# Kernel optimization log

Measured on AMD Instinct MI355X. Metric: run time of the kernel, lower is better.

Reference implementation:

```python
import jax, jax.numpy as jnp
import numpy as np

B, G, GI = 128, 360, 174          # batch, n_groups, voxels per group
EF, ET, U = 512, 512, 512         # feat embed, text embed, LSTM units
AU, VOC, T = 32, 5000, 20         # attention units, vocab, max_len


def _leaky(x):
    return jnp.where(x >= 0, x, 0.2 * x)


def _ln(x, g, b, eps=1e-5):
    m = x.mean(-1, keepdims=True)
    v = ((x - m) ** 2).mean(-1, keepdims=True)
    return (x - m) / jnp.sqrt(v + eps) * g + b


def setup_inputs() -> dict:
    key = jax.random.key(0)
    ks = jax.random.split(key, 24)
    def n(k, shape, s=0.02):
        return jax.random.normal(k, shape, jnp.float32) * s
    return {
        "features": jax.random.normal(ks[0], (B, G * GI), jnp.float32),
        "text": jax.random.randint(ks[1], (B, T), 0, VOC),
        "a0": jnp.zeros((B, U), jnp.float32),
        "c0": jnp.zeros((B, U), jnp.float32),
        "enc_W": n(ks[2], (G, GI, EF)), "enc_b": n(ks[3], (G, EF)),
        "enc_ln_g": jnp.ones((EF,), jnp.float32), "enc_ln_b": jnp.zeros((EF,), jnp.float32),
        "attn_W1": n(ks[4], (EF, AU)), "attn_b1": n(ks[5], (AU,)),
        "attn_W2": n(ks[6], (U, AU)), "attn_b2": n(ks[7], (AU,)),
        "attn_V": n(ks[8], (AU, 1)), "attn_bV": n(ks[9], (1,)),
        "emb": n(ks[10], (VOC, ET)),
        "W_ih": n(ks[11], (4 * U, EF + ET)), "W_hh": n(ks[12], (4 * U, U)),
        "b_ih": n(ks[13], (4 * U,)), "b_hh": n(ks[14], (4 * U,)),
        "ln_g": jnp.ones((U,), jnp.float32), "ln_b": jnp.zeros((U,), jnp.float32),
        "dec_W1": n(ks[15], (U, 256)), "dec_b1": n(ks[16], (256,)),
        "dec_W2": n(ks[17], (256, VOC)), "dec_b2": n(ks[18], (VOC,)),
        "subject": 0,
    }


def reference(features, text, a0, c0, enc_W, enc_b, enc_ln_g, enc_ln_b,
              attn_W1, attn_b1, attn_W2, attn_b2, attn_V, attn_bV, emb,
              W_ih, W_hh, b_ih, b_hh, ln_g, ln_b,
              dec_W1, dec_b1, dec_W2, dec_b2, subject):
    # LocallyConnected encoder (weights for the selected subject): groups are
    # 360 contiguous equal splits of the voxel axis -> gather == reshape.
    x = features.reshape(B, G, GI)
    feat = _ln(_leaky(jnp.einsum('bgi,gio->bgo', x, enc_W) + enc_b),
               enc_ln_g, enc_ln_b)                       # [B, G, EF]
    # hidden-independent half of attention, hoisted out of the recurrence
    f1 = jax.nn.relu(jnp.einsum('bge,eu->bgu', feat, attn_W1) + attn_b1)  # [B,G,AU]
    txt = emb[text]                                      # [B, T, ET]

    def step(carry, x_t):
        a, c = carry                                     # [B,U], [B,U]
        h2 = jax.nn.relu(a @ attn_W2 + attn_b2)          # [B, AU]
        score = jnp.tanh(f1 + h2[:, None, :]) @ attn_V + attn_bV  # [B,G,1]
        w = jax.nn.softmax(score, axis=1)
        ctx = jnp.sum(w * feat, axis=1)                  # [B, EF]
        xin = jnp.concatenate([ctx, x_t], axis=1)        # [B, EF+ET]
        gates = xin @ W_ih.T + a @ W_hh.T + b_ih + b_hh  # [B, 4U]
        i, f, g, o = jnp.split(gates, 4, axis=1)         # torch gate order i,f,g,o
        c = jax.nn.sigmoid(f) * c + jax.nn.sigmoid(i) * jnp.tanh(g)
        h = jax.nn.sigmoid(o) * jnp.tanh(c)
        a = _ln(_leaky(h), ln_g, ln_b)                   # fed back as LSTM hidden
        out = jax.nn.softmax(_leaky(a @ dec_W1 + dec_b1) @ dec_W2 + dec_b2, axis=-1)
        return (a, c), (out, w)

    _, (outs, ws) = jax.lax.scan(step, (a0, c0), jnp.swapaxes(txt, 0, 1))
    output = jnp.swapaxes(outs, 0, 1)                    # [B, T, VOC]
    attention_scores = jnp.swapaxes(ws, 0, 1)            # [B, T, G, 1]
    return output, attention_scores
```

## Files before the change

### kernel.cpp

```cpp
#include <hip/hip_runtime.h>
#include <stdint.h>

#define B_  128
#define G_  360
#define GI_ 174
#define EF_ 512
#define U_  512
#define AU_ 32
#define VOC_ 5000
#define T_  20

typedef short short8 __attribute__((ext_vector_type(8)));
typedef float floatx4 __attribute__((ext_vector_type(4)));

#define GLD16(gp, lp) __builtin_amdgcn_global_load_lds( \
    (const __attribute__((address_space(1))) void*)(gp), \
    (__attribute__((address_space(3))) void*)(lp), 16, 0, 0)

__device__ __forceinline__ unsigned short f2bf(float f){
  unsigned u = __float_as_uint(f);
  u += 0x7fffu + ((u>>16)&1u);
  return (unsigned short)(u>>16);
}
__device__ __forceinline__ float2 bfpair(unsigned u){
  float2 r; r.x = __uint_as_float(u<<16); r.y = __uint_as_float(u & 0xffff0000u); return r;
}
__device__ __forceinline__ unsigned packbf(float a, float b){
  return ((unsigned)f2bf(b)<<16) | (unsigned)f2bf(a);
}
__device__ __forceinline__ float sigmf(float x){ return 1.0f/(1.0f + __expf(-x)); }
__device__ __forceinline__ float tanhf_(float x){ return 1.0f - 2.0f/(1.0f + __expf(2.0f*x)); }
__device__ __forceinline__ float leaky_(float x){ return x >= 0.f ? x : 0.2f*x; }

__device__ __forceinline__ int swzcol(int cc, int e){
  return (cc & ~63) | ((((cc>>3)&7) ^ e)<<3) | (cc&7);
}

__global__ __launch_bounds__(256) void k_cvt(
    const int* __restrict__ text, const float* __restrict__ emb,
    const float* __restrict__ Wih, const float* __restrict__ Whh,
    const float* __restrict__ bih, const float* __restrict__ bhh,
    const float* __restrict__ W1, const float* __restrict__ b1,
    const float* __restrict__ encg, const float* __restrict__ encb,
    const float* __restrict__ dW1, const float* __restrict__ dW2,
    float* __restrict__ stats, unsigned short* __restrict__ Wstep,
    float* __restrict__ bias_sum, unsigned short* __restrict__ ASbuf,
    unsigned short* __restrict__ W1g, float* __restrict__ f1c,
    unsigned short* __restrict__ dW1t, unsigned short* __restrict__ dW2t)
{
  __shared__ float tile[64][65];
  const int blk = blockIdx.x, tid = threadIdx.x;
  if (blk < 90){
    int i = blk*1024 + tid*4;
    *(float4*)&stats[i] = make_float4(0.f,0.f,0.f,0.f);
  } else if (blk < 2138){
    int j = blk - 90;
    #pragma unroll
    for (int q=0;q<6;++q){
      int c = q*256 + tid;
      float v;
      if (c < 512)       v = Wih[(size_t)j*1024 + 512 + c];
      else if (c < 1024) v = Wih[(size_t)j*1024 + (c - 512)];
      else               v = Whh[(size_t)j*512 + (c - 1024)];
      int cd = c;
      if (c >= 512) cd = 512 + swzcol(c - 512, j&7);
      Wstep[(size_t)j*1536 + cd] = f2bf(v);
    }
  } else if (blk < 2146){
    int i = (blk-2138)*256 + tid;
    bias_sum[i] = bih[i] + bhh[i];
  } else if (blk < 4706){
    int r = blk - 2146; int t = r >> 7, b = r & 127;
    int idx = text[b*T_ + t];
    float2 v = *(const float2*)&emb[(size_t)idx*512 + 2*tid];
    ((unsigned*)ASbuf)[(((size_t)r*1536)>>1) + tid] = packbf(v.x, v.y);
  } else if (blk == 4706){
    if (tid < 32){
      float gw = 0.f, bw = 0.f;
      for (int k=0;k<512;++k){
        float wv = W1[(size_t)k*32 + tid];
        float gk = encg[k], bk = encb[k];
        W1g[(size_t)tid*512 + k] = f2bf(gk*wv);
        gw += gk*wv; bw += bk*wv;
      }
      f1c[tid] = gw; f1c[32+tid] = bw + b1[tid];
    }
  } else if (blk < 4739){
    int q = blk - 4707; int kt = q >> 2, nt = q & 3;
    int k0 = kt*64, n0 = nt*64;
    #pragma unroll
    for (int it=0; it<16; ++it){
      int idx = it*256 + tid; int kk = idx>>6, nn = idx&63;
      tile[kk][nn] = dW1[(size_t)(k0+kk)*256 + n0+nn];
    }
    __syncthreads();
    #pragma unroll
    for (int it=0; it<16; ++it){
      int idx = it*256 + tid; int nn = idx>>6, kk = idx&63;
      dW1t[(size_t)(n0+nn)*512 + k0+kk] = f2bf(tile[kk][nn]);
    }
  } else {
    int q = blk - 4739; int kt = q/80, nt = q - kt*80;
    int k0 = kt*64, n0 = nt*64;
    #pragma unroll
    for (int it=0; it<16; ++it){
      int idx = it*256 + tid; int kk = idx>>6, nn = idx&63;
      tile[kk][nn] = (n0+nn < VOC_) ? dW2[(size_t)(k0+kk)*VOC_ + n0+nn] : 0.f;
    }
    __syncthreads();
    #pragma unroll
    for (int it=0; it<16; ++it){
      int idx = it*256 + tid; int nn = idx>>6, kk = idx&63;
      dW2t[(size_t)(n0+nn)*256 + k0+kk] = f2bf(tile[kk][nn]);
    }
  }
}

__device__ __forceinline__ int swz64(int row, int k){
  return row*64 + ((((k>>3) ^ (row&7)))<<3) + (k&7);
}
__global__ __launch_bounds__(512) void k_enc(
    const float* __restrict__ features, const float* __restrict__ encW,
    const float* __restrict__ encB,
    unsigned short* __restrict__ ybuf, float* __restrict__ stats)
{
  __shared__ __align__(16) unsigned short As[128*64];
  __shared__ __align__(16) unsigned short Bs[128*64];
  const int g = blockIdx.y, n0 = blockIdx.x*128;
  const int tid = threadIdx.x, w = tid>>6, l = tid&63;
  const int quad = l>>4, col16 = l&15;
  const int wm = w>>1, wn = w&1;
  const int m0w = wm*32, n0w = wn*64;

  floatx4 acc[2][4];
  #pragma unroll
  for (int mi=0;mi<2;++mi)
    #pragma unroll
    for (int ni=0;ni<4;++ni)
      acc[mi][ni] = (floatx4){0.f,0.f,0.f,0.f};

  for (int c=0; c<3; ++c){
    if (c > 0) __syncthreads();
    #pragma unroll
    for (int q=0; q<4; ++q){
      int idx = q*512 + tid;
      int row = idx >> 4;
      int kl  = (idx & 15)*4;
      int kgl = c*64 + kl;
      const float* fp = features + (size_t)row*(G_*GI_) + (size_t)g*GI_ + kgl;
      float4 v;
      if (kgl + 3 < GI_){
        v = *(const float4*)fp;
      } else {
        v.x = (kgl+0 < GI_) ? fp[0] : 0.f;
        v.y = (kgl+1 < GI_) ? fp[1] : 0.f;
        v.z = (kgl+2 < GI_) ? fp[2] : 0.f;
        v.w = (kgl+3 < GI_) ? fp[3] : 0.f;
      }
      int e = row*64 + (((kl>>3) ^ (row&7))<<3) + (kl&7);
      uint2 pk; pk.x = packbf(v.x, v.y); pk.y = packbf(v.z, v.w);
      *(uint2*)&As[e] = pk;
    }
    #pragma unroll
    for (int z=0; z<8; ++z){
      int kk = (tid>>6) + 8*z;
      int k  = c*64 + kk;
      int nn = (tid&63)*2;
      if (k < GI_){
        const float* wp = encW + ((size_t)g*GI_ + k)*512 + n0 + nn;
        float2 v = *(const float2*)wp;
        Bs[swz64(nn,   kk)] = f2bf(v.x);
        Bs[swz64(nn+1, kk)] = f2bf(v.y);
      } else {
        Bs[swz64(nn,   kk)] = 0;
        Bs[swz64(nn+1, kk)] = 0;
      }
    }
    __syncthreads();
    #pragma unroll
    for (int it=0; it<2; ++it){
      int kk = it*32 + quad*8;
      short8 af[2], bfr[4];
      #pragma unroll
      for (int mi=0;mi<2;++mi){
        int row = m0w + mi*16 + col16;
        af[mi] = *(const short8*)&As[row*64 + (((kk>>3) ^ (row&7))<<3)];
      }
      #pragma unroll
      for (int ni=0;ni<4;++ni){
        int rowb = n0w + ni*16 + col16;
        bfr[ni] = *(const short8*)&Bs[rowb*64 + (((kk>>3) ^ (rowb&7))<<3)];
      }
      #pragma unroll
      for (int mi=0;mi<2;++mi)
        #pragma unroll
        for (int ni=0;ni<4;++ni)
          acc[mi][ni] = __builtin_amdgcn_mfma_f32_16x16x32_bf16(af[mi], bfr[ni], acc[mi][ni], 0,0,0);
    }
  }

  #pragma unroll
  for (int mi=0;mi<2;++mi){
    float sy[4] = {0.f,0.f,0.f,0.f};
    float sq[4] = {0.f,0.f,0.f,0.f};
    #pragma unroll
    for (int ni=0;ni<4;++ni){
      int nG = n0 + n0w + ni*16 + col16;
      float bv = encB[(size_t)g*512 + nG];
      #pragma unroll
      for (int reg=0;reg<4;++reg){
        int row = m0w + mi*16 + quad*4 + reg;
        float y = leaky_(acc[mi][ni][reg] + bv);
        unsigned short yh = f2bf(y);
        ybuf[((size_t)row*G_ + g)*512 + nG] = yh;
        float yr = __uint_as_float(((unsigned)yh)<<16);
        sy[reg] += yr; sq[reg] += yr*yr;
      }
    }
    #pragma unroll
    for (int reg=0; reg<4; ++reg){
      float a = sy[reg], bq = sq[reg];
      #pragma unroll
      for (int mk=1; mk<16; mk<<=1){ a += __shfl_xor(a, mk, 64); bq += __shfl_xor(bq, mk, 64); }
      if (col16 == 0){
        int row = m0w + mi*16 + quad*4 + reg;
        atomicAdd(&stats[((size_t)row*G_ + g)*2],     a);
        atomicAdd(&stats[((size_t)row*G_ + g)*2 + 1], bq);
      }
    }
  }
}

template<int TN, int NBK, int MODE, int KSPLIT=1>
__global__ __launch_bounds__(256) void k_gemm(
    const unsigned short* __restrict__ A, int lda,
    const unsigned short* __restrict__ Bt, int ldb,
    const float* __restrict__ bias,
    float* __restrict__ outf, unsigned short* __restrict__ outh,
    const float* __restrict__ stats, float* __restrict__ stats2,
    const float* __restrict__ f1c)
{
  constexpr int NI = TN/32;
  __shared__ __align__(16) unsigned short As[128*64];
  __shared__ __align__(16) unsigned short Bs[TN*64];
  const int tid = threadIdx.x;
  const int w = tid >> 6, l = tid & 63;
  const int n0 = blockIdx.x * TN;
  const int ks = (KSPLIT > 1) ? blockIdx.y : 0;
  const int r0 = (KSPLIT > 1) ? 0 : blockIdx.y * 128;
  const int quad = l>>4, col16 = l&15;
  const int m0w = (w>>1)*64, n0w = (w&1)*(TN/2);
  const int arow = w*32, brow = w*(TN/4);

  const unsigned short* Ag = A + (size_t)(r0 + arow + (l>>3))*lda + (l&7)*8;
  const unsigned short* Bg = Bt + (size_t)(n0 + brow + (l>>3))*ldb + (l&7)*8;

  floatx4 acc[4][NI];
  #pragma unroll
  for (int mi=0;mi<4;++mi)
    #pragma unroll
    for (int ni=0;ni<NI;++ni)
      acc[mi][ni] = (floatx4){0.f,0.f,0.f,0.f};

  for (int it=0; it<NBK; ++it){
    int k0 = (ks*NBK + it)*64;
    #pragma unroll
    for (int q=0;q<4;++q)
      GLD16(Ag + (size_t)q*8*lda + k0, As + (arow + q*8)*64);
    #pragma unroll
    for (int q=0;q<TN/32;++q)
      GLD16(Bg + (size_t)q*8*ldb + k0, Bs + (brow + q*8)*64);
    __syncthreads();
    #pragma unroll
    for (int kc=0;kc<2;++kc){
      int koff = kc*32 + quad*8;
      short8 af[4], bfr[NI];
      #pragma unroll
      for (int mi=0;mi<4;++mi)
        af[mi] = *(const short8*)&As[(m0w + mi*16 + col16)*64 + koff];
      #pragma unroll
      for (int ni=0;ni<NI;++ni)
        bfr[ni] = *(const short8*)&Bs[(n0w + ni*16 + col16)*64 + koff];
      #pragma unroll
      for (int mi=0;mi<4;++mi)
        #pragma unroll
        for (int ni=0;ni<NI;++ni)
          acc[mi][ni] = __builtin_amdgcn_mfma_f32_16x16x32_bf16(af[mi], bfr[ni], acc[mi][ni], 0,0,0);
    }
    __syncthreads();
  }

  if constexpr (MODE == 0){
    float* op = outf + (size_t)ks*(128*2048);
    #pragma unroll
    for (int ni=0; ni<NI; ++ni){
      int nG = n0 + n0w + ni*16 + col16;
      float bv = (KSPLIT == 1 || ks == 0) ? bias[nG] : 0.f;
      #pragma unroll
      for (int mi=0; mi<4; ++mi)
        #pragma unroll
        for (int reg=0; reg<4; ++reg){
          int r = r0 + m0w + mi*16 + quad*4 + reg;
          op[(size_t)r*2048 + nG] = acc[mi][ni][reg] + bv;
        }
    }
  } else if constexpr (MODE == 1){
    int nG = n0w + col16;
    float gw = f1c[nG], bwv = f1c[32+nG];
    #pragma unroll
    for (int mi=0; mi<4; ++mi)
      #pragma unroll
      for (int reg=0; reg<4; ++reg){
        int r = r0 + m0w + mi*16 + quad*4 + reg;
        float2 st = *(const float2*)&stats[(size_t)r*2];
        float m = st.x * (1.f/512.f);
        float var = st.y * (1.f/512.f) - m*m;
        float rs = rsqrtf(var + 1e-5f);
        float v = rs*(acc[mi][0][reg] - m*gw) + bwv;
        v = v > 0.f ? v : 0.f;
        outf[(size_t)r*32 + nG] = v;
        if (((w&1)==0) && col16==0){
          stats2[(size_t)r*2] = m; stats2[(size_t)r*2+1] = rs;
        }
      }
  } else if constexpr (MODE == 2){
    #pragma unroll
    for (int ni=0; ni<NI; ++ni){
      int nG = n0 + n0w + ni*16 + col16;
      float bv = bias[nG];
      #pragma unroll
      for (int mi=0; mi<4; ++mi)
        #pragma unroll
        for (int reg=0; reg<4; ++reg){
          int r = r0 + m0w + mi*16 + quad*4 + reg;
          outh[(size_t)r*256 + nG] = f2bf(leaky_(acc[mi][ni][reg] + bv));
        }
    }
  } else {
    #pragma unroll
    for (int ni=0; ni<NI; ++ni){
      int nG = n0 + n0w + ni*16 + col16;
      if (nG < VOC_){
        float bv = bias[nG];
        #pragma unroll
        for (int mi=0; mi<4; ++mi)
          #pragma unroll
          for (int reg=0; reg<4; ++reg){
            int r = r0 + m0w + mi*16 + quad*4 + reg;
            int bb = r & 127, tt = r >> 7;
            outf[((size_t)bb*T_ + tt)*VOC_ + nG] = acc[mi][ni][reg] + bv;
          }
      }
    }
  }
}

__global__ __launch_bounds__(256) void k_gates(
    const unsigned short* __restrict__ A,
    const unsigned short* __restrict__ Bt,
    float* __restrict__ outp)
{
  __shared__ __align__(16) unsigned short As[128*128];
  __shared__ __align__(16) unsigned short Bs[64*128];
  const int tid = threadIdx.x, w = tid>>6, l = tid&63;
  const int ks = blockIdx.y;
  const int n0 = blockIdx.x*64;
  const int quad = l>>4, col16 = l&15;
  const int m0w = (w>>1)*64, n0w = (w&1)*32;
  const int arow = w*32, brow = w*16;

  const unsigned short* Ag = A + (size_t)(arow + (l>>4))*1536 + ks*128 + (l&15)*8;
  const unsigned short* Bg = Bt + (size_t)(n0 + brow + (l>>4))*1536 + 512 + ks*128 + (l&15)*8;
  #pragma unroll
  for (int q=0;q<8;++q)
    GLD16(Ag + (size_t)q*4*1536, As + (arow + q*4)*128);
  #pragma unroll
  for (int q=0;q<4;++q)
    GLD16(Bg + (size_t)q*4*1536, Bs + (brow + q*4)*128);

  floatx4 acc[4][2];
  #pragma unroll
  for (int mi=0;mi<4;++mi)
    #pragma unroll
    for (int ni=0;ni<2;++ni)
      acc[mi][ni] = (floatx4){0.f,0.f,0.f,0.f};

  __syncthreads();
  #pragma unroll
  for (int kc=0;kc<4;++kc){
    int koff = kc*32 + quad*8;
    int kbase = koff & 64;
    int kx = (koff>>3)&7;
    short8 af[4], bfr[2];
    #pragma unroll
    for (int mi=0;mi<4;++mi){
      int row = m0w + mi*16 + col16;
      af[mi] = *(const short8*)&As[row*128 + kbase + ((kx ^ (row&7))<<3)];
    }
    #pragma unroll
    for (int ni=0;ni<2;++ni){
      int rowb = n0w + ni*16 + col16;
      bfr[ni] = *(const short8*)&Bs[rowb*128 + kbase + ((kx ^ (rowb&7))<<3)];
    }
    #pragma unroll
    for (int mi=0;mi<4;++mi)
      #pragma unroll
      for (int ni=0;ni<2;++ni)
        acc[mi][ni] = __builtin_amdgcn_mfma_f32_16x16x32_bf16(af[mi], bfr[ni], acc[mi][ni], 0,0,0);
  }

  float* op = outp + (size_t)ks*(128*2048);
  #pragma unroll
  for (int ni=0; ni<2; ++ni){
    int nG = n0 + n0w + ni*16 + col16;
    #pragma unroll
    for (int mi=0; mi<4; ++mi)
      #pragma unroll
      for (int reg=0; reg<4; ++reg){
        int r = m0w + mi*16 + quad*4 + reg;
        op[(size_t)r*2048 + nG] = acc[mi][ni][reg];
      }
  }
}

__global__ __launch_bounds__(256) void k_cellattn(
    const float* __restrict__ gall, const float* __restrict__ gtx,
    const float* __restrict__ c_in,
    float* __restrict__ c_out, const float* __restrict__ a0,
    const float* __restrict__ lng, const float* __restrict__ lnb,
    const float* __restrict__ W2, const float* __restrict__ b2,
    const float* __restrict__ Vv, const float* __restrict__ bV,
    const float* __restrict__ f1, const unsigned short* __restrict__ ybuf,
    const float* __restrict__ stats2,
    const float* __restrict__ encg, const float* __restrict__ encb,
    unsigned short* __restrict__ ASlot, unsigned short* __restrict__ a_bf,
    float* __restrict__ att_out, int t_att, int mode_cell, int do_attn)
{
  __shared__ float a_s[512];
  __shared__ float sc[G_];
  __shared__ float hred[8*32];
  __shared__ float h2s[32];
  __shared__ float red[16];
  __shared__ float mrs[2];
  __shared__ float2 cred[4][256];
  const int b = blockIdx.x, tid = threadIdx.x;
  const int wv = tid >> 6, ln = tid & 63;

  if (mode_cell){
    float hl2[2];
    #pragma unroll
    for (int q=0;q<2;++q){
      int u = tid + q*256;
      size_t base = (size_t)b*2048;
      float gi = gtx[base+u];
      float gf = gtx[base+512+u];
      float gc = gtx[base+1024+u];
      float go = gtx[base+1536+u];
      #pragma unroll
      for (int s=0;s<8;++s){
        const float* gp = gall + (size_t)s*(128*2048) + base;
        gi += gp[u]; gf += gp[512+u]; gc += gp[1024+u]; go += gp[1536+u];
      }
      float c = sigmf(gf)*c_in[(size_t)b*512+u] + sigmf(gi)*tanhf_(gc);
      c_out[(size_t)b*512+u] = c;
      hl2[q] = leaky_(sigmf(go)*tanhf_(c));
    }
    float s = hl2[0]+hl2[1], ss = hl2[0]*hl2[0]+hl2[1]*hl2[1];
    #pragma unroll
    for (int mk=1;mk<64;mk<<=1){ s += __shfl_xor(s,mk,64); ss += __shfl_xor(ss,mk,64); }
    if (ln==0){ red[wv]=s; red[8+wv]=ss; }
    __syncthreads();
    if (tid==0){
      float S  = red[0]+red[1]+red[2]+red[3];
      float SS = red[8]+red[9]+red[10]+red[11];
      float mean = S*(1.f/512.f);
      float var  = SS*(1.f/512.f) - mean*mean;
      mrs[0]=mean; mrs[1]=rsqrtf(var+1e-5f);
    }
    __syncthreads();
    float mean = mrs[0], rstd = mrs[1];
    #pragma unroll
    for (int q=0;q<2;++q){
      int u = tid + q*256;
      float av = (hl2[q]-mean)*rstd*lng[u] + lnb[u];
      a_s[u] = av;
      a_bf[(size_t)b*512 + u] = f2bf(av);
      if (do_attn){
        int pc = swzcol(512 + u, b&7);
        ASlot[(size_t)b*1536 + 512 + pc] = f2bf(av);
      }
    }
  } else {
    #pragma unroll
    for (int q=0;q<2;++q){
      int u = tid + q*256;
      float av = a0[(size_t)b*512 + u];
      a_s[u] = av;
      int pc = swzcol(512 + u, b&7);
      ASlot[(size_t)b*1536 + 512 + pc] = f2bf(av);
    }
  }
  __syncthreads();
  if (!do_attn) return;

  {
    int u = tid & 31, ch = tid >> 5;
    float p = 0.f;
    const float* w2p = W2 + (size_t)ch*64*32 + u;
    const float* ap = a_s + ch*64;
    #pragma unroll 8
    for (int e=0;e<64;++e) p += ap[e]*w2p[(size_t)e*32];
    hred[ch*32+u] = p;
  }
  __syncthreads();
  if (tid < 32){
    float p = hred[tid];
    #pragma unroll
    for (int ch=1; ch<8; ++ch) p += hred[ch*32+tid];
    p += b2[tid];
    h2s[tid] = p>0.f? p:0.f;
  }
  __syncthreads();
  float bVv = bV[0];
  for (int gg = tid; gg < G_; gg += 256){
    const float* fp = f1 + ((size_t)b*G_ + gg)*32;
    float s = bVv;
    #pragma unroll
    for (int u=0;u<32;++u) s += tanhf_(fp[u] + h2s[u]) * Vv[u];
    sc[gg] = s;
  }
  __syncthreads();
  float mx = -1e30f;
  for (int gg=tid; gg<G_; gg+=256) mx = fmaxf(mx, sc[gg]);
  #pragma unroll
  for (int mk=1;mk<64;mk<<=1) mx = fmaxf(mx, __shfl_xor(mx,mk,64));
  if (ln==0) red[wv]=mx;
  __syncthreads();
  if (tid==0) red[0] = fmaxf(fmaxf(red[0],red[1]),fmaxf(red[2],red[3]));
  __syncthreads();
  mx = red[0];
  float psum = 0.f;
  for (int gg=tid; gg<G_; gg+=256){
    float e = __expf(sc[gg]-mx);
    sc[gg] = e; psum += e;
  }
  #pragma unroll
  for (int mk=1;mk<64;mk<<=1) psum += __shfl_xor(psum,mk,64);
  if (ln==0) red[8+wv]=psum;
  __syncthreads();
  if (tid==0) red[8] = red[8]+red[9]+red[10]+red[11];
  __syncthreads();
  float inv = 1.f/red[8];
  float Mop = 0.f;
  float* wout = att_out + ((size_t)b*T_ + t_att)*G_;
  for (int gg=tid; gg<G_; gg+=256){
    float wg = sc[gg]*inv;
    wout[gg] = wg;
    float2 st = *(const float2*)&stats2[((size_t)b*G_+gg)*2];
    sc[gg] = wg*st.y;
    Mop += wg*st.x*st.y;
  }
  #pragma unroll
  for (int mk=1;mk<64;mk<<=1) Mop += __shfl_xor(Mop,mk,64);
  if (ln==0) red[4+wv] = Mop;
  __syncthreads();
  if (tid==0) mrs[0] = red[4]+red[5]+red[6]+red[7];
  __syncthreads();
  float Mo = mrs[0];
  {
    const unsigned* fp = (const unsigned*)ybuf + ((size_t)b*G_)*256;
    float2 cacc[4];
    #pragma unroll
    for (int k=0;k<4;++k) cacc[k] = make_float2(0.f,0.f);
    int g0 = wv*90;
    for (int gg=g0; gg<g0+90; ++gg){
      float wq = sc[gg];
      #pragma unroll
      for (int k=0;k<4;++k){
        float2 p = bfpair(fp[(size_t)gg*256 + ln + 64*k]);
        cacc[k].x += wq*p.x; cacc[k].y += wq*p.y;
      }
    }
    #pragma unroll
    for (int k=0;k<4;++k) cred[wv][ln + 64*k] = cacc[k];
  }
  __syncthreads();
  {
    float c0v = cred[0][tid].x + cred[1][tid].x + cred[2][tid].x + cred[3][tid].x;
    float c1v = cred[0][tid].y + cred[1][tid].y + cred[2][tid].y + cred[3][tid].y;
    int e0 = 2*tid;
    float ctx0 = encg[e0]  *(c0v - Mo) + encb[e0];
    float ctx1 = encg[e0+1]*(c1v - Mo) + encb[e0+1];
    int pc = swzcol(2*tid, b&7);
    ((unsigned*)ASlot)[((size_t)b*1536 + 512 + pc)>>1] = packbf(ctx0, ctx1);
  }
}

__global__ __launch_bounds__(256) void k_softmax(float* __restrict__ outp)
{
  __shared__ float red[8];
  const size_t row = (size_t)blockIdx.x * VOC_;
  const int tid = threadIdx.x;
  const int wv = tid >> 6, ln = tid & 63;
  float v[20];
  float mx = -1e30f;
  #pragma unroll
  for (int k=0;k<20;++k){
    int idx = tid + k*256;
    v[k] = (idx < VOC_) ? outp[row+idx] : -1e30f;
    mx = fmaxf(mx, v[k]);
  }
  #pragma unroll
  for (int mk=1;mk<64;mk<<=1) mx = fmaxf(mx,__shfl_xor(mx,mk,64));
  if (ln==0) red[wv] = mx;
  __syncthreads();
  if (tid==0) red[0]=fmaxf(fmaxf(red[0],red[1]),fmaxf(red[2],red[3]));
  __syncthreads();
  mx = red[0];
  float s=0.f;
  #pragma unroll
  for (int k=0;k<20;++k){ v[k] = __expf(v[k]-mx); s += v[k]; }
  #pragma unroll
  for (int mk=1;mk<64;mk<<=1) s += __shfl_xor(s,mk,64);
  if (ln==0) red[4+wv]=s;
  __syncthreads();
  if (tid==0) red[4]=red[4]+red[5]+red[6]+red[7];
  __syncthreads();
  float inv = 1.f/red[4];
  #pragma unroll
  for (int k=0;k<20;++k){
    int idx = tid + k*256;
    if (idx < VOC_) outp[row+idx] = v[k]*inv;
  }
}

extern "C" void kernel_launch(void* const* d_in, const int* in_sizes, int n_in,
                              void* d_out, int out_size, void* d_ws, size_t ws_size,
                              hipStream_t stream) {
  const float* features = (const float*)d_in[0];
  const int*   text     = (const int*)d_in[1];
  const float* a0    = (const float*)d_in[2];
  const float* c0    = (const float*)d_in[3];
  const float* encW  = (const float*)d_in[4];
  const float* encB  = (const float*)d_in[5];
  const float* encLNg= (const float*)d_in[6];
  const float* encLNb= (const float*)d_in[7];
  const float* attnW1= (const float*)d_in[8];
  const float* attnb1= (const float*)d_in[9];
  const float* attnW2= (const float*)d_in[10];
  const float* attnb2= (const float*)d_in[11];
  const float* attnV = (const float*)d_in[12];
  const float* attnbV= (const float*)d_in[13];
  const float* emb   = (const float*)d_in[14];
  const float* Wih   = (const float*)d_in[15];
  const float* Whh   = (const float*)d_in[16];
  const float* bih   = (const float*)d_in[17];
  const float* bhh   = (const float*)d_in[18];
  const float* lng   = (const float*)d_in[19];
  const float* lnb   = (const float*)d_in[20];
  const float* dW1   = (const float*)d_in[21];
  const float* db1   = (const float*)d_in[22];
  const float* dW2   = (const float*)d_in[23];
  const float* db2   = (const float*)d_in[24];

  uint8_t* w8 = (uint8_t*)d_ws;
  unsigned short* ybuf   = (unsigned short*)(w8);
  float*          stats  = (float*)(w8 + 47185920);
  float*          stats2 = (float*)(w8 + 47554560);
  float*          f1b    = (float*)(w8 + 47923200);
  unsigned short* ASbuf  = (unsigned short*)(w8 + 53821440);
  unsigned short* Wstep  = (unsigned short*)(w8 + 61685760);
  float*          bias_sum=(float*)(w8 + 67977216);
  unsigned short* W1g    = (unsigned short*)(w8 + 67985408);
  float*          f1c    = (float*)(w8 + 68018176);
  unsigned short* dW1t   = (unsigned short*)(w8 + 68018432);
  unsigned short* dW2t   = (unsigned short*)(w8 + 68280576);
  float*          cws    = (float*)(w8 + 71950592);
  unsigned short* a_bf   = (unsigned short*)(w8 + 72212736);
  unsigned short* d1bf   = (unsigned short*)(w8 + 74834176);

  float* outp = (float*)d_out;
  float* att  = outp + 12800000;
  float* gsplit = outp;
  float* gtxt   = outp + 8*128*2048;

  hipLaunchKernelGGL(k_cvt, dim3(5059), dim3(256), 0, stream,
                     text, emb, Wih, Whh, bih, bhh, attnW1, attnb1,
                     encLNg, encLNb, dW1, dW2,
                     stats, Wstep, bias_sum, ASbuf, W1g, f1c, dW1t, dW2t);
  hipLaunchKernelGGL(k_enc, dim3(4,360), dim3(512), 0, stream,
                     features, encW, encB, ybuf, stats);
  hipLaunchKernelGGL((k_gemm<64,8,0>), dim3(32,20), dim3(256), 0, stream,
                     ASbuf, 1536, Wstep, 1536, bias_sum,
                     gtxt, (unsigned short*)nullptr,
                     (const float*)nullptr, (float*)nullptr, (const float*)nullptr);
  hipLaunchKernelGGL((k_gemm<32,8,1>), dim3(1,360), dim3(256), 0, stream,
                     ybuf, 512, W1g, 512, (const float*)nullptr,
                     f1b, (unsigned short*)nullptr, stats, stats2, f1c);
  hipLaunchKernelGGL(k_cellattn, dim3(128), dim3(256), 0, stream,
                     gsplit, gtxt, c0, cws, a0, lng, lnb, attnW2, attnb2, attnV, attnbV,
                     f1b, ybuf, stats2, encLNg, encLNb,
                     ASbuf, a_bf, att, 0, 0, 1);
  for (int t=0; t<T_; ++t){
    hipLaunchKernelGGL(k_gates, dim3(32,8), dim3(256), 0, stream,
                       ASbuf + (size_t)t*128*1536 + 512, Wstep, gsplit);
    int da = (t < T_-1) ? 1 : 0;
    unsigned short* slot = ASbuf + (size_t)((t+1 < T_) ? (t+1) : 0)*128*1536;
    hipLaunchKernelGGL(k_cellattn, dim3(128), dim3(256), 0, stream,
                       gsplit, gtxt + (size_t)t*128*2048, (t==0)?c0:cws, cws, a0, lng, lnb,
                       attnW2, attnb2, attnV, attnbV,
                       f1b, ybuf, stats2, encLNg, encLNb,
                       slot, a_bf + (size_t)t*128*512, att, t+1, 1, da);
  }
  hipLaunchKernelGGL((k_gemm<128,8,2>), dim3(2,20), dim3(256), 0, stream,
                     a_bf, 512, dW1t, 512, db1,
                     (float*)nullptr, d1bf, (const float*)nullptr, (float*)nullptr,
                     (const float*)nullptr);
  hipLaunchKernelGGL((k_gemm<128,4,3>), dim3(40,20), dim3(256), 0, stream,
                     d1bf, 256, dW2t, 256, db2,
                     outp, (unsigned short*)nullptr, (const float*)nullptr,
                     (float*)nullptr, (const float*)nullptr);
  hipLaunchKernelGGL(k_softmax, dim3(2560), dim3(256), 0, stream, outp);
}
```

Baseline: 1.011 ms.

## Vectorize weight conversion and retile encoder GEMM into smaller 64x64 blocks

The weight-packing section of the conversion kernel now has each thread load eight floats with float4 loads and store them as one 16-byte bf16 vector, with the swizzle applied per 8-element chunk. This cuts that section from 2048 blocks to 256. The encoder GEMM moves from 128x128 tiles with 512 threads to 64x64 tiles with 256 threads, launching 16x360 blocks instead of 4x360, to raise occupancy and parallelism. The cost is that each features and weight element is loaded and converted more times across blocks, and more atomic stat updates are issued.

```diff
diff --git a/kernel.cpp b/kernel.cpp
--- a/kernel.cpp
+++ b/kernel.cpp
@@ -53,28 +53,43 @@
   if (blk < 90){
     int i = blk*1024 + tid*4;
     *(float4*)&stats[i] = make_float4(0.f,0.f,0.f,0.f);
-  } else if (blk < 2138){
-    int j = blk - 90;
-    #pragma unroll
-    for (int q=0;q<6;++q){
-      int c = q*256 + tid;
-      float v;
-      if (c < 512)       v = Wih[(size_t)j*1024 + 512 + c];
-      else if (c < 1024) v = Wih[(size_t)j*1024 + (c - 512)];
-      else               v = Whh[(size_t)j*512 + (c - 1024)];
-      int cd = c;
-      if (c >= 512) cd = 512 + swzcol(c - 512, j&7);
-      Wstep[(size_t)j*1536 + cd] = f2bf(v);
-    }
-  } else if (blk < 2146){
-    int i = (blk-2138)*256 + tid;
+  } else if (blk < 346){
+    int j = (blk - 90)*8 + (tid >> 5);
+    int e = j & 7;
+    #pragma unroll
+    for (int z=0; z<6; ++z){
+      int c0 = ((tid & 31) + 32*z)*8;
+      float4 v0, v1;
+      if (c0 < 512){
+        v0 = *(const float4*)&Wih[(size_t)j*1024 + 512 + c0];
+        v1 = *(const float4*)&Wih[(size_t)j*1024 + 512 + c0 + 4];
+      } else if (c0 < 1024){
+        v0 = *(const float4*)&Wih[(size_t)j*1024 + (c0 - 512)];
+        v1 = *(const float4*)&Wih[(size_t)j*1024 + (c0 - 512) + 4];
+      } else {
+        v0 = *(const float4*)&Whh[(size_t)j*512 + (c0 - 1024)];
+        v1 = *(const float4*)&Whh[(size_t)j*512 + (c0 - 1024) + 4];
+      }
+      uint4 pk;
+      pk.x = packbf(v0.x, v0.y); pk.y = packbf(v0.z, v0.w);
+      pk.z = packbf(v1.x, v1.y); pk.w = packbf(v1.z, v1.w);
+      int cd0;
+      if (c0 < 512) cd0 = c0;
+      else {
+        int cc = c0 - 512;
+        cd0 = 512 + ((cc & ~63) | ((((cc>>3)&7) ^ e)<<3));
+      }
+      *(uint4*)&Wstep[(size_t)j*1536 + cd0] = pk;
+    }
+  } else if (blk < 354){
+    int i = (blk-346)*256 + tid;
     bias_sum[i] = bih[i] + bhh[i];
-  } else if (blk < 4706){
-    int r = blk - 2146; int t = r >> 7, b = r & 127;
+  } else if (blk < 2914){
+    int r = blk - 354; int t = r >> 7, b = r & 127;
     int idx = text[b*T_ + t];
     float2 v = *(const float2*)&emb[(size_t)idx*512 + 2*tid];
     ((unsigned*)ASbuf)[(((size_t)r*1536)>>1) + tid] = packbf(v.x, v.y);
-  } else if (blk == 4706){
+  } else if (blk == 2914){
     if (tid < 32){
       float gw = 0.f, bw = 0.f;
       for (int k=0;k<512;++k){
@@ -85,8 +100,8 @@
       }
       f1c[tid] = gw; f1c[32+tid] = bw + b1[tid];
     }
-  } else if (blk < 4739){
-    int q = blk - 4707; int kt = q >> 2, nt = q & 3;
+  } else if (blk < 2947){
+    int q = blk - 2915; int kt = q >> 2, nt = q & 3;
     int k0 = kt*64, n0 = nt*64;
     #pragma unroll
     for (int it=0; it<16; ++it){
@@ -100,7 +115,7 @@
       dW1t[(size_t)(n0+nn)*512 + k0+kk] = f2bf(tile[kk][nn]);
     }
   } else {
-    int q = blk - 4739; int kt = q/80, nt = q - kt*80;
+    int q = blk - 2947; int kt = q/80, nt = q - kt*80;
     int k0 = kt*64, n0 = nt*64;
     #pragma unroll
     for (int it=0; it<16; ++it){
@@ -119,35 +134,35 @@
 __device__ __forceinline__ int swz64(int row, int k){
   return row*64 + ((((k>>3) ^ (row&7)))<<3) + (k&7);
 }
-__global__ __launch_bounds__(512) void k_enc(
+__global__ __launch_bounds__(256) void k_enc(
     const float* __restrict__ features, const float* __restrict__ encW,
     const float* __restrict__ encB,
     unsigned short* __restrict__ ybuf, float* __restrict__ stats)
 {
-  __shared__ __align__(16) unsigned short As[128*64];
-  __shared__ __align__(16) unsigned short Bs[128*64];
-  const int g = blockIdx.y, n0 = blockIdx.x*128;
+  __shared__ __align__(16) unsigned short As[64*64];
+  __shared__ __align__(16) unsigned short Bs[64*64];
+  const int g = blockIdx.y;
+  const int m0 = (blockIdx.x >> 3)*64, n0 = (blockIdx.x & 7)*64;
   const int tid = threadIdx.x, w = tid>>6, l = tid&63;
   const int quad = l>>4, col16 = l&15;
-  const int wm = w>>1, wn = w&1;
-  const int m0w = wm*32, n0w = wn*64;
-
-  floatx4 acc[2][4];
+  const int m0w = (w>>1)*32, n0w = (w&1)*32;
+
+  floatx4 acc[2][2];
   #pragma unroll
   for (int mi=0;mi<2;++mi)
     #pragma unroll
-    for (int ni=0;ni<4;++ni)
+    for (int ni=0;ni<2;++ni)
       acc[mi][ni] = (floatx4){0.f,0.f,0.f,0.f};
 
   for (int c=0; c<3; ++c){
     if (c > 0) __syncthreads();
     #pragma unroll
     for (int q=0; q<4; ++q){
-      int idx = q*512 + tid;
+      int idx = q*256 + tid;
       int row = idx >> 4;
       int kl  = (idx & 15)*4;
       int kgl = c*64 + kl;
-      const float* fp = features + (size_t)row*(G_*GI_) + (size_t)g*GI_ + kgl;
+      const float* fp = features + (size_t)(m0+row)*(G_*GI_) + (size_t)g*GI_ + kgl;
       float4 v;
       if (kgl + 3 < GI_){
         v = *(const float4*)fp;
@@ -163,9 +178,9 @@
     }
     #pragma unroll
     for (int z=0; z<8; ++z){
-      int kk = (tid>>6) + 8*z;
+      int kk = (tid>>5) + 8*z;
       int k  = c*64 + kk;
-      int nn = (tid&63)*2;
+      int nn = (tid&31)*2;
       if (k < GI_){
         const float* wp = encW + ((size_t)g*GI_ + k)*512 + n0 + nn;
         float2 v = *(const float2*)wp;
@@ -180,21 +195,21 @@
     #pragma unroll
     for (int it=0; it<2; ++it){
       int kk = it*32 + quad*8;
-      short8 af[2], bfr[4];
+      short8 af[2], bfr[2];
       #pragma unroll
       for (int mi=0;mi<2;++mi){
         int row = m0w + mi*16 + col16;
         af[mi] = *(const short8*)&As[row*64 + (((kk>>3) ^ (row&7))<<3)];
       }
       #pragma unroll
-      for (int ni=0;ni<4;++ni){
+      for (int ni=0;ni<2;++ni){
         int rowb = n0w + ni*16 + col16;
         bfr[ni] = *(const short8*)&Bs[rowb*64 + (((kk>>3) ^ (rowb&7))<<3)];
       }
       #pragma unroll
       for (int mi=0;mi<2;++mi)
         #pragma unroll
-        for (int ni=0;ni<4;++ni)
+        for (int ni=0;ni<2;++ni)
           acc[mi][ni] = __builtin_amdgcn_mfma_f32_16x16x32_bf16(af[mi], bfr[ni], acc[mi][ni], 0,0,0);
     }
   }
@@ -204,12 +219,12 @@
     float sy[4] = {0.f,0.f,0.f,0.f};
     float sq[4] = {0.f,0.f,0.f,0.f};
     #pragma unroll
-    for (int ni=0;ni<4;++ni){
+    for (int ni=0;ni<2;++ni){
       int nG = n0 + n0w + ni*16 + col16;
       float bv = encB[(size_t)g*512 + nG];
       #pragma unroll
       for (int reg=0;reg<4;++reg){
-        int row = m0w + mi*16 + quad*4 + reg;
+        int row = m0 + m0w + mi*16 + quad*4 + reg;
         float y = leaky_(acc[mi][ni][reg] + bv);
         unsigned short yh = f2bf(y);
         ybuf[((size_t)row*G_ + g)*512 + nG] = yh;
@@ -223,7 +238,7 @@
       #pragma unroll
       for (int mk=1; mk<16; mk<<=1){ a += __shfl_xor(a, mk, 64); bq += __shfl_xor(bq, mk, 64); }
       if (col16 == 0){
-        int row = m0w + mi*16 + quad*4 + reg;
+        int row = m0 + m0w + mi*16 + quad*4 + reg;
         atomicAdd(&stats[((size_t)row*G_ + g)*2],     a);
         atomicAdd(&stats[((size_t)row*G_ + g)*2 + 1], bq);
       }
@@ -684,11 +699,11 @@
   float* gsplit = outp;
   float* gtxt   = outp + 8*128*2048;
 
-  hipLaunchKernelGGL(k_cvt, dim3(5059), dim3(256), 0, stream,
+  hipLaunchKernelGGL(k_cvt, dim3(3267), dim3(256), 0, stream,
                      text, emb, Wih, Whh, bih, bhh, attnW1, attnb1,
                      encLNg, encLNb, dW1, dW2,
                      stats, Wstep, bias_sum, ASbuf, W1g, f1c, dW1t, dW2t);
-  hipLaunchKernelGGL(k_enc, dim3(4,360), dim3(512), 0, stream,
+  hipLaunchKernelGGL(k_enc, dim3(16,360), dim3(256), 0, stream,
                      features, encW, encB, ybuf, stats);
   hipLaunchKernelGGL((k_gemm<64,8,0>), dim3(32,20), dim3(256), 0, stream,
                      ASbuf, 1536, Wstep, 1536, bias_sum,
```

After: 1.069 ms. +5.7%, slower.
